# Performance work log

Hardware: AMD Instinct MI355X
Metric: run time of the kernel (lower is better)

The kernel has to match this reference:

```python
import jax, jax.numpy as jnp
import numpy as np

DICT_LEN = 9
NUM_LS = 8
DIM = 1024
SEQ = 2048
BZ = 32


def setup_inputs() -> dict:
    key = jax.random.key(0)
    k_x, k_ids, k_w, k_b = jax.random.split(key, 4)
    x = jax.random.normal(k_x, (SEQ, BZ, DIM), dtype=jnp.float32)
    lang_ids = jax.random.randint(k_ids, (BZ,), 0, DICT_LEN)
    # torch nn.Linear init: U(-1/sqrt(in), 1/sqrt(in)), weight shape [out, in]
    bound = 1.0 / np.sqrt(DIM)
    W = jax.random.uniform(k_w, (NUM_LS, DIM, DIM), dtype=jnp.float32, minval=-bound, maxval=bound)
    b = jax.random.uniform(k_b, (NUM_LS, DIM), dtype=jnp.float32, minval=-bound, maxval=bound)
    return {"x": x, "lang_ids": lang_ids, "W": W, "b": b}


def reference(x, lang_ids, W, b):
    # Mapper.forward: gid = dict_len - 1 - lang_ids; tokens with gid in [1, num_ls]
    # are transformed by Linear #(gid-1); all other batch columns pass through.
    gid = DICT_LEN - 1 - lang_ids                      # [bz]
    active = (gid >= 1) & (gid <= NUM_LS)              # [bz]
    eidx = jnp.clip(gid - 1, 0, NUM_LS - 1)            # [bz] expert index (dummy 0 where inactive)
    We = W[eidx]                                       # [bz, dim, dim] (torch Linear weight layout [out, in])
    be = b[eidx]                                       # [bz, dim]
    y = jnp.einsum("sbd,bed->sbe", x, We) + be[None, :, :]
    return jnp.where(active[None, :, None], y, x)
```

## Files before the change

### kernel.cpp

```cpp
#include <hip/hip_runtime.h>
#include <hip/hip_bf16.h>

#define TSEQ 2048
#define TBZ  32
#define TDIM 1024
#define NLS  8

typedef __attribute__((ext_vector_type(8))) short bf16x8;
typedef __attribute__((ext_vector_type(4))) float f32x4;

__device__ inline unsigned int pk2(float lo, float hi) {
    __hip_bfloat162 h = __float22bfloat162_rn(make_float2(lo, hi));
    return *reinterpret_cast<const unsigned int*>(&h);
}

__device__ inline void gload_lds16(const void* g, void* l) {
    __builtin_amdgcn_global_load_lds(
        (const __attribute__((address_space(1))) unsigned int*)g,
        (__attribute__((address_space(3))) unsigned int*)l,
        16, 0, 0);
}

__global__ __launch_bounds__(256) void conv_x(const float* __restrict__ x,
                                              unsigned short* __restrict__ xb) {
    const int total = TSEQ * TBZ * TDIM / 8;
    const int stride = gridDim.x * 256;
    for (int i = blockIdx.x * 256 + threadIdx.x; i < total; i += stride) {
        const int d8  = i & (TDIM / 8 - 1);
        const int row = i >> 7;
        const int s   = row >> 5;
        const int b   = row & (TBZ - 1);
        const float* src = x + (long)row * TDIM + d8 * 8;
        f32x4 v0 = *(const f32x4*)(src);
        f32x4 v1 = *(const f32x4*)(src + 4);
        uint4 o;
        o.x = pk2(v0.x, v0.y); o.y = pk2(v0.z, v0.w);
        o.z = pk2(v1.x, v1.y); o.w = pk2(v1.z, v1.w);
        *(uint4*)(xb + (long)(b * TSEQ + s) * TDIM + d8 * 8) = o;
    }
}

__global__ __launch_bounds__(256) void conv_w(const float* __restrict__ W,
                                              unsigned short* __restrict__ wb) {
    const int total = NLS * TDIM * TDIM / 8;
    const int stride = gridDim.x * 256;
    for (int i = blockIdx.x * 256 + threadIdx.x; i < total; i += stride) {
        const float* src = W + (long)i * 8;
        f32x4 v0 = *(const f32x4*)(src);
        f32x4 v1 = *(const f32x4*)(src + 4);
        uint4 o;
        o.x = pk2(v0.x, v0.y); o.y = pk2(v0.z, v0.w);
        o.z = pk2(v1.x, v1.y); o.w = pk2(v1.z, v1.w);
        *(uint4*)(wb + (long)i * 8) = o;
    }
}


#define BAR __builtin_amdgcn_s_barrier()
#define LGKM asm volatile("s_waitcnt lgkmcnt(0)" ::: "memory")
#define VMC(n) asm volatile("s_waitcnt vmcnt(" #n ")" ::: "memory")
#define KAo(kv) (((kv) & 1023) + (((kv) >> 10) << 18))
#define KBo(kv) ((kv) & 1023)

__global__ __launch_bounds__(512, 2) void mapper_gemm8p(
    const unsigned short* __restrict__ xb,
    const int* __restrict__ lang_ids,
    const unsigned short* __restrict__ wb,
    const float* __restrict__ bias,
    const float* __restrict__ x,
    float* __restrict__ out)
{
    const int p  = blockIdx.x;
    const int l  = (p & 7) * 64 + (p >> 3);
    const int b  = l >> 4;
    const int strip = (l >> 2) & 3;
    const int nt = l & 3;
    const int s0 = strip * 512;
    const int e0 = nt * 256;
    const int tid = threadIdx.x;

    const int gid = 8 - lang_ids[b];
    if (!(gid >= 1 && gid <= 8)) {
        const f32x4* xs = (const f32x4*)x;
        f32x4*       os = (f32x4*)out;
        const int rs4 = TBZ * TDIM / 4;
        for (int i = tid; i < 512 * 256 / 4; i += 512) {
            int r = i >> 6;
            int c = i & 63;
            long idx = (long)(s0 + r) * rs4 + b * (TDIM / 4) + (e0 >> 2) + c;
            os[idx] = xs[idx];
        }
        return;
    }
    const int eb = gid - 1;

    __shared__ uint4 ldsbuf[131072 / 16];
    char* ldsc = (char*)ldsbuf;

    const int lane = tid & 63;
    const int wave = tid >> 6;
    const int wr   = wave >> 2;
    const int wc   = wave & 3;
    const int fr   = lane & 15;
    const int fq   = lane >> 4;
    const int fr7  = fr & 7;

    const unsigned short* __restrict__ Aab = xb + (long)b  * TSEQ * TDIM + (long)s0 * TDIM;
    const unsigned short* __restrict__ Bbb = wb + (long)eb * TDIM * TDIM + (long)e0 * TDIM;

    const int L    = lane;
    const int lch8 = ((L & 7) ^ (L >> 3)) * 8;
    const int ldA0 = wave * 2048 + L * 16;
    const unsigned short* aG[2][2];
    const unsigned short* bG[2][2];
    #pragma unroll
    for (int j = 0; j < 2; ++j) {
        const int rr = wave * 16 + j * 8 + (L >> 3);
        #pragma unroll
        for (int mh = 0; mh < 2; ++mh)
            aG[j][mh] = Aab + ((rr >> 6) * 128 + mh * 64 + (rr & 63)) * TDIM + lch8;
        #pragma unroll
        for (int nh = 0; nh < 2; ++nh)
            bG[j][nh] = Bbb + ((rr >> 5) * 64 + nh * 32 + (rr & 31)) * TDIM + lch8;
    }

#define STAGE_A(slot, mh, kofs) do { \
    gload_lds16(aG[0][mh] + (kofs), ldsc + (slot)*32768 + (mh)*16384 + ldA0); \
    gload_lds16(aG[1][mh] + (kofs), ldsc + (slot)*32768 + (mh)*16384 + ldA0 + 1024); \
} while (0)
#define STAGE_B(slot, nh, kofs) do { \
    gload_lds16(bG[0][nh] + (kofs), ldsc + 65536 + (slot)*32768 + (nh)*16384 + ldA0); \
    gload_lds16(bG[1][nh] + (kofs), ldsc + 65536 + (slot)*32768 + (nh)*16384 + ldA0 + 1024); \
} while (0)
#define RD_A(slot, mh) do { \
    _Pragma("unroll") for (int ml = 0; ml < 4; ++ml) { \
        const int rr = wr * 64 + ml * 16 + fr; \
        _Pragma("unroll") for (int kk = 0; kk < 2; ++kk) \
            af[ml][kk] = *(const bf16x8*)(ldsc + (slot)*32768 + (mh)*16384 + rr*128 + (((kk*4+fq) ^ fr7) << 4)); \
    } } while (0)
#define RD_B(slot, nh, br) do { \
    _Pragma("unroll") for (int nl = 0; nl < 2; ++nl) { \
        const int rr = wc * 32 + nl * 16 + fr; \
        _Pragma("unroll") for (int kk = 0; kk < 2; ++kk) \
            br[nl][kk] = *(const bf16x8*)(ldsc + 65536 + (slot)*32768 + (nh)*16384 + rr*128 + (((kk*4+fq) ^ fr7) << 4)); \
    } } while (0)
#define MM(mh, nh, br) do { \
    __builtin_amdgcn_s_setprio(1); \
    _Pragma("unroll") for (int ml = 0; ml < 4; ++ml) \
    _Pragma("unroll") for (int nl = 0; nl < 2; ++nl) \
    _Pragma("unroll") for (int kk = 0; kk < 2; ++kk) \
        acc[(mh)*4+ml][(nh)*2+nl] = __builtin_amdgcn_mfma_f32_16x16x32_bf16( \
            br[nl][kk], af[ml][kk], acc[(mh)*4+ml][(nh)*2+nl], 0, 0, 0); \
    __builtin_amdgcn_s_setprio(0); \
} while (0)

    f32x4 acc[8][4];
    #pragma unroll
    for (int m = 0; m < 8; ++m)
        #pragma unroll
        for (int n = 0; n < 4; ++n)
            acc[m][n] = (f32x4){0.f, 0.f, 0.f, 0.f};

    bf16x8 af[4][2], bf0[2][2], bf1[2][2];

    STAGE_A(0, 0, 0);  STAGE_B(0, 0, 0);  STAGE_B(0, 1, 0);  STAGE_A(0, 1, 0);
    STAGE_A(1, 0, 64); STAGE_B(1, 0, 64); STAGE_B(1, 1, 64);
    VMC(6); BAR;

    const int cs  = lane & 15;
    const int eqb = (lane >> 4) << 2;

    for (int mtl = 0; mtl < 2; ++mtl) {
        for (int it = 0; it < 8; ++it) {
            const int kva = mtl * 1024 + it * 128;
            const int kb = kva + 64;
            const int kn = kva + 128;
            const int km = kva + 192;
            RD_A(0, 0); RD_B(0, 0, bf0); STAGE_A(1, 1, KAo(kb));
            BAR; LGKM; MM(0, 0, bf0); BAR;
            RD_B(0, 1, bf1); STAGE_A(0, 0, KAo(kn));
            BAR; LGKM; MM(0, 1, bf1); BAR;
            RD_A(0, 1); STAGE_B(0, 0, KBo(kn));
            BAR; LGKM; MM(1, 0, bf0); BAR;
            STAGE_B(0, 1, KBo(kn));
            BAR; MM(1, 1, bf1); VMC(6); BAR;
            RD_A(1, 0); RD_B(1, 0, bf0); STAGE_A(0, 1, KAo(kn));
            BAR; LGKM; MM(0, 0, bf0); BAR;
            RD_B(1, 1, bf1); STAGE_A(1, 0, KAo(km));
            BAR; LGKM; MM(0, 1, bf1); BAR;
            RD_A(1, 1); STAGE_B(1, 0, KBo(km));
            BAR; LGKM; MM(1, 0, bf0); BAR;
            STAGE_B(1, 1, KBo(km));
            BAR; MM(1, 1, bf1); VMC(6); BAR;
        }

        const int sb = s0 + mtl * 256 + wr * 128;
        #pragma unroll
        for (int n = 0; n < 4; ++n) {
            const int e = e0 + wc * 64 + n * 16 + eqb;
            const f32x4 bv4 = *(const f32x4*)&bias[eb * TDIM + e];
            #pragma unroll
            for (int m = 0; m < 8; ++m) {
                const int s = sb + m * 16 + cs;
                *(f32x4*)&out[(long)s * (TBZ * TDIM) + b * TDIM + e] = acc[m][n] + bv4;
            }
        }
        #pragma unroll
        for (int m = 0; m < 8; ++m)
            #pragma unroll
            for (int n = 0; n < 4; ++n)
                acc[m][n] = (f32x4){0.f, 0.f, 0.f, 0.f};
    }
#undef STAGE_A
#undef STAGE_B
#undef RD_A
#undef RD_B
#undef MM
}

__device__ inline unsigned short f2bf(float f) {
    union { float f; unsigned int u; } v; v.f = f;
    unsigned int r = v.u + 0x7fffu + ((v.u >> 16) & 1u);
    return (unsigned short)(r >> 16);
}
constexpr int FLDS = 40;

__global__ __launch_bounds__(256) void mapper_fused(
    const float* __restrict__ x, const int* __restrict__ lang_ids,
    const float* __restrict__ W, const float* __restrict__ bias,
    float* __restrict__ out)
{
    const int bid = blockIdx.x;
    const int b   = bid >> 7;
    const int t   = bid & 127;
    const int mt  = t >> 3;
    const int nt  = t & 7;
    const int s0  = mt * 128;
    const int e0  = nt * 128;
    const int tid = threadIdx.x;

    const int gid = 8 - lang_ids[b];
    const bool active = (gid >= 1) && (gid <= 8);
    int eb = gid - 1; eb = eb < 0 ? 0 : (eb > 7 ? 7 : eb);

    if (!active) {
        const f32x4* xs = (const f32x4*)x;
        f32x4*       os = (f32x4*)out;
        const int rs4 = TBZ * TDIM / 4;
        for (int i = tid; i < 128 * 128 / 4; i += 256) {
            int r = i >> 5, c = i & 31;
            long idx = (long)(s0 + r) * rs4 + b * (TDIM / 4) + (e0 >> 2) + c;
            os[idx] = xs[idx];
        }
        return;
    }

    __shared__ unsigned short As[128 * FLDS];
    __shared__ unsigned short Bs[128 * FLDS];
    const float* __restrict__ Wb = W + (long)eb * TDIM * TDIM;

    const int lane = tid & 63;
    const int wave = tid >> 6;
    const int wrr  = wave >> 1;
    const int wcc  = wave & 1;

    f32x4 acc[4][4];
    #pragma unroll
    for (int m = 0; m < 4; ++m)
        #pragma unroll
        for (int n = 0; n < 4; ++n)
            acc[m][n] = (f32x4){0.f, 0.f, 0.f, 0.f};

    const int rg = tid >> 3;
    const int cg = tid & 7;
    const int fr = lane & 15;
    const int fo = (lane >> 4) * 8;

    for (int k0 = 0; k0 < TDIM; k0 += 32) {
        __syncthreads();
        #pragma unroll
        for (int pp = 0; pp < 4; ++pp) {
            const int r = rg + pp * 32;
            f32x4 av = *(const f32x4*)(x  + (long)(s0 + r) * (TBZ * TDIM) + b * TDIM + k0 + cg * 4);
            f32x4 bv = *(const f32x4*)(Wb + (long)(e0 + r) * TDIM + k0 + cg * 4);
            unsigned int alo = (unsigned)f2bf(av.x) | ((unsigned)f2bf(av.y) << 16);
            unsigned int ahi = (unsigned)f2bf(av.z) | ((unsigned)f2bf(av.w) << 16);
            unsigned int blo = (unsigned)f2bf(bv.x) | ((unsigned)f2bf(bv.y) << 16);
            unsigned int bhi = (unsigned)f2bf(bv.z) | ((unsigned)f2bf(bv.w) << 16);
            *(uint2*)&As[r * FLDS + cg * 4] = make_uint2(alo, ahi);
            *(uint2*)&Bs[r * FLDS + cg * 4] = make_uint2(blo, bhi);
        }
        __syncthreads();

        bf16x8 af2[4], bfm[4];
        #pragma unroll
        for (int m = 0; m < 4; ++m)
            af2[m] = *(const bf16x8*)&As[(wrr * 64 + m * 16 + fr) * FLDS + fo];
        #pragma unroll
        for (int n = 0; n < 4; ++n)
            bfm[n] = *(const bf16x8*)&Bs[(wcc * 64 + n * 16 + fr) * FLDS + fo];
        #pragma unroll
        for (int m = 0; m < 4; ++m)
            #pragma unroll
            for (int n = 0; n < 4; ++n)
                acc[m][n] = __builtin_amdgcn_mfma_f32_16x16x32_bf16(af2[m], bfm[n], acc[m][n], 0, 0, 0);
    }

    const int cr = lane >> 4;
    const int cc2 = lane & 15;
    #pragma unroll
    for (int n = 0; n < 4; ++n) {
        const int e  = e0 + wcc * 64 + n * 16 + cc2;
        const float bv = bias[eb * TDIM + e];
        #pragma unroll
        for (int m = 0; m < 4; ++m) {
            #pragma unroll
            for (int j = 0; j < 4; ++j) {
                const int s = s0 + wrr * 64 + m * 16 + cr * 4 + j;
                out[(long)s * (TBZ * TDIM) + b * TDIM + e] = acc[m][n][j] + bv;
            }
        }
    }
}

extern "C" void kernel_launch(void* const* d_in, const int* in_sizes, int n_in,
                              void* d_out, int out_size, void* d_ws, size_t ws_size,
                              hipStream_t stream) {
    const float* x        = (const float*)d_in[0];
    const int*   lang_ids = (const int*)d_in[1];
    const float* W        = (const float*)d_in[2];
    const float* bias     = (const float*)d_in[3];
    float*       out      = (float*)d_out;

    const size_t xbytes = (size_t)TSEQ * TBZ * TDIM * 2;
    const size_t wbytes = (size_t)NLS * TDIM * TDIM * 2;

    if (ws_size >= xbytes + wbytes) {
        unsigned short* xbp = (unsigned short*)d_ws;
        unsigned short* wbp = (unsigned short*)((char*)d_ws + xbytes);
        conv_x<<<4096, 256, 0, stream>>>(x, xbp);
        conv_w<<<2048, 256, 0, stream>>>(W, wbp);
        mapper_gemm8p<<<512, 512, 0, stream>>>(xbp, lang_ids, wbp, bias, x, out);
    } else {
        mapper_fused<<<TBZ * 16 * 8, 256, 0, stream>>>(x, lang_ids, W, bias, out);
    }
}
```

Baseline: 260.4 us.

## Fuse x fp32-to-bf16 conversion into GEMM A-operand staging

Removes the separate conv_x pass and the bf16 copy of x in workspace. The GEMM now loads fp32 x rows straight into registers, packs them to bf16 and writes them to swizzled LDS, with a register prefetch one k-step ahead synchronised by vmcnt waits. This saves a full read and write of the 256MB activation tensor, but the GEMM now reads twice as many A bytes from global memory, and A staging goes through registers and VALU packing instead of direct-to-LDS loads.

```diff
diff --git a/kernel.cpp b/kernel.cpp
--- a/kernel.cpp
+++ b/kernel.cpp
@@ -19,25 +19,6 @@
         (const __attribute__((address_space(1))) unsigned int*)g,
         (__attribute__((address_space(3))) unsigned int*)l,
         16, 0, 0);
-}
-
-__global__ __launch_bounds__(256) void conv_x(const float* __restrict__ x,
-                                              unsigned short* __restrict__ xb) {
-    const int total = TSEQ * TBZ * TDIM / 8;
-    const int stride = gridDim.x * 256;
-    for (int i = blockIdx.x * 256 + threadIdx.x; i < total; i += stride) {
-        const int d8  = i & (TDIM / 8 - 1);
-        const int row = i >> 7;
-        const int s   = row >> 5;
-        const int b   = row & (TBZ - 1);
-        const float* src = x + (long)row * TDIM + d8 * 8;
-        f32x4 v0 = *(const f32x4*)(src);
-        f32x4 v1 = *(const f32x4*)(src + 4);
-        uint4 o;
-        o.x = pk2(v0.x, v0.y); o.y = pk2(v0.z, v0.w);
-        o.z = pk2(v1.x, v1.y); o.w = pk2(v1.z, v1.w);
-        *(uint4*)(xb + (long)(b * TSEQ + s) * TDIM + d8 * 8) = o;
-    }
 }
 
 __global__ __launch_bounds__(256) void conv_w(const float* __restrict__ W,
@@ -59,15 +40,14 @@
 #define BAR __builtin_amdgcn_s_barrier()
 #define LGKM asm volatile("s_waitcnt lgkmcnt(0)" ::: "memory")
 #define VMC(n) asm volatile("s_waitcnt vmcnt(" #n ")" ::: "memory")
-#define KAo(kv) (((kv) & 1023) + (((kv) >> 10) << 18))
+#define FENCE asm volatile("" ::: "memory")
 #define KBo(kv) ((kv) & 1023)
 
-__global__ __launch_bounds__(512, 2) void mapper_gemm8p(
-    const unsigned short* __restrict__ xb,
+__global__ __launch_bounds__(512, 2) void mapper_gemm8f(
+    const float* __restrict__ x,
     const int* __restrict__ lang_ids,
     const unsigned short* __restrict__ wb,
     const float* __restrict__ bias,
-    const float* __restrict__ x,
     float* __restrict__ out)
 {
     const int p  = blockIdx.x;
@@ -105,29 +85,49 @@
     const int fq   = lane >> 4;
     const int fr7  = fr & 7;
 
-    const unsigned short* __restrict__ Aab = xb + (long)b  * TSEQ * TDIM + (long)s0 * TDIM;
     const unsigned short* __restrict__ Bbb = wb + (long)eb * TDIM * TDIM + (long)e0 * TDIM;
 
     const int L    = lane;
     const int lch8 = ((L & 7) ^ (L >> 3)) * 8;
     const int ldA0 = wave * 2048 + L * 16;
-    const unsigned short* aG[2][2];
+    int sRowA[2];
     const unsigned short* bG[2][2];
     #pragma unroll
     for (int j = 0; j < 2; ++j) {
         const int rr = wave * 16 + j * 8 + (L >> 3);
-        #pragma unroll
-        for (int mh = 0; mh < 2; ++mh)
-            aG[j][mh] = Aab + ((rr >> 6) * 128 + mh * 64 + (rr & 63)) * TDIM + lch8;
+        sRowA[j] = s0 + (rr >> 6) * 128 + (rr & 63);
         #pragma unroll
         for (int nh = 0; nh < 2; ++nh)
             bG[j][nh] = Bbb + ((rr >> 5) * 64 + nh * 32 + (rr & 31)) * TDIM + lch8;
     }
 
-#define STAGE_A(slot, mh, kofs) do { \
-    gload_lds16(aG[0][mh] + (kofs), ldsc + (slot)*32768 + (mh)*16384 + ldA0); \
-    gload_lds16(aG[1][mh] + (kofs), ldsc + (slot)*32768 + (mh)*16384 + ldA0 + 1024); \
+#define ISSUE_A(kv) do { \
+    const int kvc_ = ((kv) < 2048) ? (kv) : 0; \
+    const int radv_ = (kvc_ >> 10) << 8; \
+    const int kof_ = (kvc_ & 1023); \
+    _Pragma("unroll") for (int j = 0; j < 2; ++j) { \
+        const float* s_ = x + (long)(sRowA[j] + radv_) * (TBZ * TDIM) + b * TDIM + kof_ + lch8; \
+        ar[j*2+0] = *(const f32x4*)(s_); \
+        ar[j*2+1] = *(const f32x4*)(s_ + 4); \
+    } \
+    FENCE; \
+    _Pragma("unroll") for (int j = 0; j < 2; ++j) { \
+        const float* s_ = x + (long)(sRowA[j] + radv_ + 64) * (TBZ * TDIM) + b * TDIM + kof_ + lch8; \
+        ar[4+j*2+0] = *(const f32x4*)(s_); \
+        ar[4+j*2+1] = *(const f32x4*)(s_ + 4); \
+    } \
 } while (0)
+
+#define COMMIT_A(slot, mh) do { \
+    _Pragma("unroll") for (int j = 0; j < 2; ++j) { \
+        f32x4 p0_ = ar[(mh)*4 + j*2], p1_ = ar[(mh)*4 + j*2 + 1]; \
+        uint4 w_; \
+        w_.x = pk2(p0_.x, p0_.y); w_.y = pk2(p0_.z, p0_.w); \
+        w_.z = pk2(p1_.x, p1_.y); w_.w = pk2(p1_.z, p1_.w); \
+        *(uint4*)(ldsc + (slot)*32768 + (mh)*16384 + ldA0 + j*1024) = w_; \
+    } \
+} while (0)
+
 #define STAGE_B(slot, nh, kofs) do { \
     gload_lds16(bG[0][nh] + (kofs), ldsc + 65536 + (slot)*32768 + (nh)*16384 + ldA0); \
     gload_lds16(bG[1][nh] + (kofs), ldsc + 65536 + (slot)*32768 + (nh)*16384 + ldA0 + 1024); \
@@ -161,11 +161,18 @@
         for (int n = 0; n < 4; ++n)
             acc[m][n] = (f32x4){0.f, 0.f, 0.f, 0.f};
 
+    f32x4  ar[8];
     bf16x8 af[4][2], bf0[2][2], bf1[2][2];
 
-    STAGE_A(0, 0, 0);  STAGE_B(0, 0, 0);  STAGE_B(0, 1, 0);  STAGE_A(0, 1, 0);
-    STAGE_A(1, 0, 64); STAGE_B(1, 0, 64); STAGE_B(1, 1, 64);
-    VMC(6); BAR;
+    ISSUE_A(0);
+    FENCE;
+    STAGE_B(0, 0, 0); STAGE_B(0, 1, 0); STAGE_B(1, 0, 64); STAGE_B(1, 1, 64);
+    VMC(8);
+    COMMIT_A(0, 0); COMMIT_A(0, 1);
+    ISSUE_A(64);
+    VMC(0);
+    COMMIT_A(1, 0); COMMIT_A(1, 1);
+    LGKM; BAR;
 
     const int cs  = lane & 15;
     const int eqb = (lane >> 4) << 2;
@@ -173,25 +180,24 @@
     for (int mtl = 0; mtl < 2; ++mtl) {
         for (int it = 0; it < 8; ++it) {
             const int kva = mtl * 1024 + it * 128;
-            const int kb = kva + 64;
             const int kn = kva + 128;
             const int km = kva + 192;
-            RD_A(0, 0); RD_B(0, 0, bf0); STAGE_A(1, 1, KAo(kb));
+            RD_A(0, 0); RD_B(0, 0, bf0); ISSUE_A(kn);
             BAR; LGKM; MM(0, 0, bf0); BAR;
-            RD_B(0, 1, bf1); STAGE_A(0, 0, KAo(kn));
+            RD_B(0, 1, bf1);
             BAR; LGKM; MM(0, 1, bf1); BAR;
-            RD_A(0, 1); STAGE_B(0, 0, KBo(kn));
+            RD_A(0, 1); VMC(4); COMMIT_A(0, 0); STAGE_B(0, 0, KBo(kn));
             BAR; LGKM; MM(1, 0, bf0); BAR;
-            STAGE_B(0, 1, KBo(kn));
-            BAR; MM(1, 1, bf1); VMC(6); BAR;
-            RD_A(1, 0); RD_B(1, 0, bf0); STAGE_A(0, 1, KAo(kn));
+            VMC(2); COMMIT_A(0, 1); STAGE_B(0, 1, KBo(kn));
+            BAR; MM(1, 1, bf1); BAR;
+            RD_A(1, 0); RD_B(1, 0, bf0); ISSUE_A(km);
             BAR; LGKM; MM(0, 0, bf0); BAR;
-            RD_B(1, 1, bf1); STAGE_A(1, 0, KAo(km));
+            RD_B(1, 1, bf1);
             BAR; LGKM; MM(0, 1, bf1); BAR;
-            RD_A(1, 1); STAGE_B(1, 0, KBo(km));
+            RD_A(1, 1); VMC(4); COMMIT_A(1, 0); STAGE_B(1, 0, KBo(km));
             BAR; LGKM; MM(1, 0, bf0); BAR;
-            STAGE_B(1, 1, KBo(km));
-            BAR; MM(1, 1, bf1); VMC(6); BAR;
+            VMC(2); COMMIT_A(1, 1); STAGE_B(1, 1, KBo(km));
+            BAR; MM(1, 1, bf1); BAR;
         }
 
         const int sb = s0 + mtl * 256 + wr * 128;
@@ -211,7 +217,8 @@
             for (int n = 0; n < 4; ++n)
                 acc[m][n] = (f32x4){0.f, 0.f, 0.f, 0.f};
     }
-#undef STAGE_A
+#undef ISSUE_A
+#undef COMMIT_A
 #undef STAGE_B
 #undef RD_A
 #undef RD_B
@@ -332,15 +339,12 @@
     const float* bias     = (const float*)d_in[3];
     float*       out      = (float*)d_out;
 
-    const size_t xbytes = (size_t)TSEQ * TBZ * TDIM * 2;
     const size_t wbytes = (size_t)NLS * TDIM * TDIM * 2;
 
-    if (ws_size >= xbytes + wbytes) {
-        unsigned short* xbp = (unsigned short*)d_ws;
-        unsigned short* wbp = (unsigned short*)((char*)d_ws + xbytes);
-        conv_x<<<4096, 256, 0, stream>>>(x, xbp);
+    if (ws_size >= wbytes) {
+        unsigned short* wbp = (unsigned short*)d_ws;
         conv_w<<<2048, 256, 0, stream>>>(W, wbp);
-        mapper_gemm8p<<<512, 512, 0, stream>>>(xbp, lang_ids, wbp, bias, x, out);
+        mapper_gemm8f<<<512, 512, 0, stream>>>(x, lang_ids, wbp, bias, out);
     } else {
         mapper_fused<<<TBZ * 16 * 8, 256, 0, stream>>>(x, lang_ids, W, bias, out);
     }
```

Result: slower. 305.4 us (+17.3%).

## Move passthrough copy into conversion kernel and enlarge GEMM sequence strips

Applied to the files above, without the earlier changes.

The x-to-bf16 conversion kernel now reads lang_ids per batch column. For inactive columns it writes the fp32 passthrough directly to the output instead of converting, so the GEMM kernel no longer rereads x for those columns. The GEMM grid is halved: each block covers a 1024-row sequence strip (the M loop runs 4 times instead of 2), which gives fewer blocks and more weight-tile reuse per block. The risk is that 256 blocks is close to the CU count, so load balance and tail effects may get worse when some columns are inactive.

```diff
diff --git a/kernel.cpp b/kernel.cpp
--- a/kernel.cpp
+++ b/kernel.cpp
@@ -21,22 +21,32 @@
         16, 0, 0);
 }
 
-__global__ __launch_bounds__(256) void conv_x(const float* __restrict__ x,
-                                              unsigned short* __restrict__ xb) {
-    const int total = TSEQ * TBZ * TDIM / 8;
-    const int stride = gridDim.x * 256;
-    for (int i = blockIdx.x * 256 + threadIdx.x; i < total; i += stride) {
-        const int d8  = i & (TDIM / 8 - 1);
-        const int row = i >> 7;
-        const int s   = row >> 5;
-        const int b   = row & (TBZ - 1);
-        const float* src = x + (long)row * TDIM + d8 * 8;
+__global__ __launch_bounds__(256) void conv_x(
+    const float* __restrict__ x, const int* __restrict__ lang_ids,
+    unsigned short* __restrict__ xb, float* __restrict__ out)
+{
+    const int b   = blockIdx.x >> 5;
+    const int s0c = (blockIdx.x & 31) * 64;
+    const int gid = 8 - lang_ids[b];
+    const bool active = (gid >= 1) && (gid <= 8);
+
+    for (int i = threadIdx.x; i < 64 * 128; i += 256) {
+        const int ls = i >> 7;
+        const int d8 = i & 127;
+        const int s  = s0c + ls;
+        const float* src = x + ((long)s * TBZ + b) * TDIM + d8 * 8;
         f32x4 v0 = *(const f32x4*)(src);
         f32x4 v1 = *(const f32x4*)(src + 4);
-        uint4 o;
-        o.x = pk2(v0.x, v0.y); o.y = pk2(v0.z, v0.w);
-        o.z = pk2(v1.x, v1.y); o.w = pk2(v1.z, v1.w);
-        *(uint4*)(xb + (long)(b * TSEQ + s) * TDIM + d8 * 8) = o;
+        if (active) {
+            uint4 o;
+            o.x = pk2(v0.x, v0.y); o.y = pk2(v0.z, v0.w);
+            o.z = pk2(v1.x, v1.y); o.w = pk2(v1.z, v1.w);
+            *(uint4*)(xb + ((long)b * TSEQ + s) * TDIM + d8 * 8) = o;
+        } else {
+            float* dst = out + ((long)s * TBZ + b) * TDIM + d8 * 8;
+            *(f32x4*)(dst)     = v0;
+            *(f32x4*)(dst + 4) = v1;
+        }
     }
 }
 
@@ -67,31 +77,19 @@
     const int* __restrict__ lang_ids,
     const unsigned short* __restrict__ wb,
     const float* __restrict__ bias,
-    const float* __restrict__ x,
     float* __restrict__ out)
 {
     const int p  = blockIdx.x;
-    const int l  = (p & 7) * 64 + (p >> 3);
-    const int b  = l >> 4;
-    const int strip = (l >> 2) & 3;
+    const int l  = (p & 7) * 32 + (p >> 3);
+    const int b  = l >> 3;
+    const int strip = (l >> 2) & 1;
     const int nt = l & 3;
-    const int s0 = strip * 512;
+    const int s0 = strip * 1024;
     const int e0 = nt * 256;
     const int tid = threadIdx.x;
 
     const int gid = 8 - lang_ids[b];
-    if (!(gid >= 1 && gid <= 8)) {
-        const f32x4* xs = (const f32x4*)x;
-        f32x4*       os = (f32x4*)out;
-        const int rs4 = TBZ * TDIM / 4;
-        for (int i = tid; i < 512 * 256 / 4; i += 512) {
-            int r = i >> 6;
-            int c = i & 63;
-            long idx = (long)(s0 + r) * rs4 + b * (TDIM / 4) + (e0 >> 2) + c;
-            os[idx] = xs[idx];
-        }
-        return;
-    }
+    if (!(gid >= 1 && gid <= 8)) return;
     const int eb = gid - 1;
 
     __shared__ uint4 ldsbuf[131072 / 16];
@@ -170,7 +168,7 @@
     const int cs  = lane & 15;
     const int eqb = (lane >> 4) << 2;
 
-    for (int mtl = 0; mtl < 2; ++mtl) {
+    for (int mtl = 0; mtl < 4; ++mtl) {
         for (int it = 0; it < 8; ++it) {
             const int kva = mtl * 1024 + it * 128;
             const int kb = kva + 64;
@@ -338,9 +336,9 @@
     if (ws_size >= xbytes + wbytes) {
         unsigned short* xbp = (unsigned short*)d_ws;
         unsigned short* wbp = (unsigned short*)((char*)d_ws + xbytes);
-        conv_x<<<4096, 256, 0, stream>>>(x, xbp);
+        conv_x<<<1024, 256, 0, stream>>>(x, lang_ids, xbp, out);
         conv_w<<<2048, 256, 0, stream>>>(W, wbp);
-        mapper_gemm8p<<<512, 512, 0, stream>>>(xbp, lang_ids, wbp, bias, x, out);
+        mapper_gemm8p<<<256, 512, 0, stream>>>(xbp, lang_ids, wbp, bias, out);
     } else {
         mapper_fused<<<TBZ * 16 * 8, 256, 0, stream>>>(x, lang_ids, W, bias, out);
     }
```

New measurement: 265.9 us. 2.1% more time.
